# Optimization experiments

Hardware: AMD Instinct MI355X
Metric: run time of the kernel (lower is better)

The kernel has to match this reference:

```python
import jax, jax.numpy as jnp
import numpy as np


def setup_inputs() -> dict:
    key = jax.random.key(0)
    ks = jax.random.split(key, 5)
    B, T, I, H = 64, 2048, 128, 128
    bound = 1.0 / np.sqrt(H)
    x = jax.random.normal(ks[0], (B, T, I), dtype=jnp.float32)
    W_xh = jax.random.uniform(ks[1], (H, I), minval=-bound, maxval=bound, dtype=jnp.float32)
    b_xh = jax.random.uniform(ks[2], (H,), minval=-bound, maxval=bound, dtype=jnp.float32)
    W_hh = jax.random.uniform(ks[3], (H, H), minval=-bound, maxval=bound, dtype=jnp.float32)
    b_hh = jax.random.uniform(ks[4], (H,), minval=-bound, maxval=bound, dtype=jnp.float32)
    return {"x": x, "W_xh": W_xh, "b_xh": b_xh, "W_hh": W_hh, "b_hh": b_hh}


def reference(x, W_xh, b_xh, W_hh, b_hh):
    # x: [B, T, I]; nn.Linear applies x @ W.T + b.
    # Precompute the input projection for all timesteps in one GEMM.
    xp = jnp.einsum('bti,hi->bth', x, W_xh) + b_xh  # [B, T, H]
    B = x.shape[0]
    H = W_hh.shape[0]
    h0 = jnp.zeros((B, H), dtype=x.dtype)

    def step(h, xt):
        h_new = jnp.tanh(xt + h @ W_hh.T + b_hh)
        return h_new, h_new

    h_last, hs = jax.lax.scan(step, h0, jnp.swapaxes(xp, 0, 1))  # hs: [T, B, H]
    h_seq = jnp.swapaxes(hs, 0, 1)  # [B, T, H]
    return h_seq, h_last[None]  # h: [1, B, H]
```

## Files before the change

kernel.cpp:

```cpp
#include <hip/hip_runtime.h>

#define B_ 64
#define T_ 2048
#define I_ 128
#define H_ 128
#define CHUNK 128
#define NCHUNK (T_ / CHUNK)

typedef _Float16 f16x8 __attribute__((ext_vector_type(8)));
typedef float    f32x4 __attribute__((ext_vector_type(4)));
typedef int      i32x4 __attribute__((ext_vector_type(4)));

__global__ __launch_bounds__(256) void xp_gemm(
    const float* __restrict__ x, const float* __restrict__ Wxh,
    const float* __restrict__ bxh, const float* __restrict__ bhh,
    float* __restrict__ xp)
{
    __shared__ float ws[H_ * I_];
    const int tid = threadIdx.x;
    {
        const float4* src = (const float4*)Wxh;
        float4* dst = (float4*)ws;
        #pragma unroll
        for (int i = 0; i < (H_ * I_ / 4) / 256; ++i)
            dst[tid + i * 256] = src[tid + i * 256];
    }
    __syncthreads();

    const int r0 = (tid >> 4) * 8;
    const int c0 = (tid & 15) * 8;
    const float* xb = x + ((size_t)blockIdx.x * 128 + r0) * I_;
    const float* wb = ws + c0 * I_;

    float acc[8][8];
    #pragma unroll
    for (int i = 0; i < 8; ++i)
        #pragma unroll
        for (int j = 0; j < 8; ++j) acc[i][j] = 0.f;

    float4 xa[8], wa[8], xn[8], wn[8];
    #pragma unroll
    for (int i = 0; i < 8; ++i) xa[i] = *(const float4*)(xb + i * I_);
    #pragma unroll
    for (int j = 0; j < 8; ++j) wa[j] = *(const float4*)(wb + j * I_);

    for (int k4 = 0; k4 < 32; k4 += 2) {
        #pragma unroll
        for (int i = 0; i < 8; ++i) xn[i] = *(const float4*)(xb + i * I_ + k4 * 4 + 4);
        #pragma unroll
        for (int j = 0; j < 8; ++j) wn[j] = *(const float4*)(wb + j * I_ + k4 * 4 + 4);
        #pragma unroll
        for (int i = 0; i < 8; ++i)
            #pragma unroll
            for (int j = 0; j < 8; ++j) {
                acc[i][j] = fmaf(xa[i].x, wa[j].x, acc[i][j]);
                acc[i][j] = fmaf(xa[i].y, wa[j].y, acc[i][j]);
                acc[i][j] = fmaf(xa[i].z, wa[j].z, acc[i][j]);
                acc[i][j] = fmaf(xa[i].w, wa[j].w, acc[i][j]);
            }
        if (k4 + 2 < 32) {
            #pragma unroll
            for (int i = 0; i < 8; ++i) xa[i] = *(const float4*)(xb + i * I_ + k4 * 4 + 8);
            #pragma unroll
            for (int j = 0; j < 8; ++j) wa[j] = *(const float4*)(wb + j * I_ + k4 * 4 + 8);
        }
        #pragma unroll
        for (int i = 0; i < 8; ++i)
            #pragma unroll
            for (int j = 0; j < 8; ++j) {
                acc[i][j] = fmaf(xn[i].x, wn[j].x, acc[i][j]);
                acc[i][j] = fmaf(xn[i].y, wn[j].y, acc[i][j]);
                acc[i][j] = fmaf(xn[i].z, wn[j].z, acc[i][j]);
                acc[i][j] = fmaf(xn[i].w, wn[j].w, acc[i][j]);
            }
    }

    const float4 ba0 = *(const float4*)(bxh + c0);
    const float4 ba1 = *(const float4*)(bxh + c0 + 4);
    const float4 bb0 = *(const float4*)(bhh + c0);
    const float4 bb1 = *(const float4*)(bhh + c0 + 4);
    float* orow = xp + ((size_t)blockIdx.x * 128 + r0) * H_ + c0;
    #pragma unroll
    for (int i = 0; i < 8; ++i) {
        float4 o0, o1;
        o0.x = acc[i][0] + ba0.x + bb0.x; o0.y = acc[i][1] + ba0.y + bb0.y;
        o0.z = acc[i][2] + ba0.z + bb0.z; o0.w = acc[i][3] + ba0.w + bb0.w;
        o1.x = acc[i][4] + ba1.x + bb1.x; o1.y = acc[i][5] + ba1.y + bb1.y;
        o1.z = acc[i][6] + ba1.z + bb1.z; o1.w = acc[i][7] + ba1.w + bb1.w;
        *(float4*)(orow + i * H_) = o0;
        *(float4*)(orow + i * H_ + 4) = o1;
    }
}

__device__ __forceinline__ void stage_chunk64(const float* __restrict__ g,
                                              float* l, int ln)
{
    #pragma unroll
    for (int i = 0; i < 64; ++i) {
        const int off = i * 256;
        __builtin_amdgcn_global_load_lds(
            (const __attribute__((address_space(1))) unsigned int*)(g + off + ln * 4),
            (__attribute__((address_space(3))) unsigned int*)(l + off),
            16, 0, 0);
    }
}

#define FORALL(M) \
  M(0,0) M(1,0) M(2,0) M(3,0)  M(0,1) M(1,1) M(2,1) M(3,1) \
  M(0,2) M(1,2) M(2,2) M(3,2)  M(0,3) M(1,3) M(2,3) M(3,3) \
  M(0,4) M(1,4) M(2,4) M(3,4)  M(0,5) M(1,5) M(2,5) M(3,5) \
  M(0,6) M(1,6) M(2,6) M(3,6)  M(0,7) M(1,7) M(2,7) M(3,7)

#define DECLB(q,n) i32x4 bf_##q##_##n;
#define LOADB(q,n) { \
    const float* wr_ = Whh + (size_t)((n)*16 + c15) * H_ + (q)*32 + grp*8; \
    const float4 u0_ = *(const float4*)wr_; \
    const float4 u1_ = *(const float4*)(wr_ + 4); \
    f16x8 t_; \
    t_[0]=(_Float16)u0_.x; t_[1]=(_Float16)u0_.y; t_[2]=(_Float16)u0_.z; t_[3]=(_Float16)u0_.w; \
    t_[4]=(_Float16)u1_.x; t_[5]=(_Float16)u1_.y; t_[6]=(_Float16)u1_.z; t_[7]=(_Float16)u1_.w; \
    bf_##q##_##n = __builtin_bit_cast(i32x4, t_); }
#define PINB(q,n) asm volatile("" : "+a"(bf_##q##_##n));

#define FORN(M) M(0) M(1) M(2) M(3) M(4) M(5) M(6) M(7)
#define TILE(n) \
  f32x4 acc##n = __builtin_amdgcn_mfma_f32_16x16x32_f16(a0, __builtin_bit_cast(f16x8, bf_0_##n), zc, 0, 0, 0); \
  acc##n = __builtin_amdgcn_mfma_f32_16x16x32_f16(a1, __builtin_bit_cast(f16x8, bf_1_##n), acc##n, 0, 0, 0); \
  acc##n = __builtin_amdgcn_mfma_f32_16x16x32_f16(a2, __builtin_bit_cast(f16x8, bf_2_##n), acc##n, 0, 0, 0); \
  acc##n = __builtin_amdgcn_mfma_f32_16x16x32_f16(a3, __builtin_bit_cast(f16x8, bf_3_##n), acc##n, 0, 0, 0);

__global__ __launch_bounds__(64) void rnn_scan(
    const float* __restrict__ Whh,
    float* __restrict__ seq , float* __restrict__ hlast)
{
    __shared__ float xpl[2][CHUNK * H_];
    __shared__ _Float16 hA[H_], hB[H_];

    const int l   = threadIdx.x;
    const int b   = blockIdx.x;
    const int c15 = l & 15;
    const int grp = l >> 4;
    const int c0  = grp * 32 + c15;
    const int c1  = c0 + 16;

    FORALL(DECLB)
    FORALL(LOADB)
    FORALL(PINB)

    hA[2 * l] = (_Float16)0.f;
    hA[2 * l + 1] = (_Float16)0.f;

    const f32x4 zc = {0.f, 0.f, 0.f, 0.f};

    float* xp = seq + (size_t)b * T_ * H_;
    stage_chunk64(xp, &xpl[0][0], l);

    auto step = [&](const _Float16* hr, _Float16* hw,
                    const float* xrow, float* sqrow) {
        const float xv0 = xrow[c0];
        const float xv1 = xrow[c1];
        const f16x8 a0 = *(const f16x8*)(hr + grp * 8);
        const f16x8 a1 = *(const f16x8*)(hr + 32 + grp * 8);
        const f16x8 a2 = *(const f16x8*)(hr + 64 + grp * 8);
        const f16x8 a3 = *(const f16x8*)(hr + 96 + grp * 8);
        FORN(TILE)
        const float r0 = grp == 0 ? acc0.x : grp == 1 ? acc2.x : grp == 2 ? acc4.x : acc6.x;
        const float r1 = grp == 0 ? acc1.x : grp == 1 ? acc3.x : grp == 2 ? acc5.x : acc7.x;
        const float p0 = r0 + xv0;
        const float p1 = r1 + xv1;
        const float e0 = exp2f(p0 * 2.8853900817779268f);
        const float e1 = exp2f(p1 * 2.8853900817779268f);
        const float h0 = 1.f - 2.f * __builtin_amdgcn_rcpf(e0 + 1.f);
        const float h1 = 1.f - 2.f * __builtin_amdgcn_rcpf(e1 + 1.f);
        hw[c0] = (_Float16)h0;
        hw[c1] = (_Float16)h1;
        const float s0 = (float)hw[2 * l];
        const float s1 = (float)hw[2 * l + 1];
        *(float2*)(sqrow + 2 * l) = make_float2(s0, s1);
    };

    for (int c = 0; c < NCHUNK; ++c) {
        asm volatile("s_waitcnt vmcnt(0)" ::: "memory");
        if (c + 1 < NCHUNK)
            stage_chunk64(xp + (size_t)(c + 1) * CHUNK * H_, &xpl[(c + 1) & 1][0], l);

        const float* xb = &xpl[c & 1][0];
        float* sq = xp + (size_t)c * CHUNK * H_;

        for (int t = 0; t < CHUNK; t += 2) {
            step(hA, hB, xb + (size_t)t * H_, sq + (size_t)t * H_);
            step(hB, hA, xb + (size_t)(t + 1) * H_, sq + (size_t)(t + 1) * H_);
        }
    }
    const float f0 = (float)hA[2 * l];
    const float f1 = (float)hA[2 * l + 1];
    *(float2*)&hlast[b * H_ + 2 * l] = make_float2(f0, f1);
}

extern "C" void kernel_launch(void* const* d_in, const int* in_sizes, int n_in,
                              void* d_out, int out_size, void* d_ws, size_t ws_size,
                              hipStream_t stream)
{
    const float* x   = (const float*)d_in[0];
    const float* Wxh = (const float*)d_in[1];
    const float* bxh = (const float*)d_in[2];
    const float* Whh = (const float*)d_in[3];
    const float* bhh = (const float*)d_in[4];
    float* out   = (float*)d_out;
    float* hlast = out + (size_t)B_ * T_ * H_;

    xp_gemm<<<(B_ * T_) / 128, 256, 0, stream>>>(x, Wxh, bxh, bhh, out);
    rnn_scan<<<B_, 64, 0, stream>>>(Whh, out, hlast);
}
```

Measured before the change: 1.174 ms.

## Transpose recurrent MFMA so W_hh is A operand and accumulate into preloaded xp

The recurrent step now computes W_hh·h with W_hh in the A operand held in AGPRs, and h as a packed f16 B vector. xp rows are loaded straight into the MFMA accumulators, which removes the separate add. Each lane gets its two outputs through a fixed permutation (P/Lw), and a single packed 32-bit write into a tiny shared buffer carries h to the next step. The output is stored as fp32 without an f16 round trip, and the step loop is no longer unrolled by two. This aims to cut LDS traffic and scalar work on the serial critical path, at the cost of inline-asm register constraints and a complex index mapping.

```diff
diff --git a/kernel.cpp b/kernel.cpp
--- a/kernel.cpp
+++ b/kernel.cpp
@@ -7,9 +7,8 @@
 #define CHUNK 128
 #define NCHUNK (T_ / CHUNK)
 
-typedef _Float16 f16x8 __attribute__((ext_vector_type(8)));
-typedef float    f32x4 __attribute__((ext_vector_type(4)));
-typedef int      i32x4 __attribute__((ext_vector_type(4)));
+typedef float f32x4 __attribute__((ext_vector_type(4)));
+typedef int   i32x4 __attribute__((ext_vector_type(4)));
 
 __global__ __launch_bounds__(256) void xp_gemm(
     const float* __restrict__ x, const float* __restrict__ Wxh,
@@ -105,79 +104,52 @@
     }
 }
 
-#define FORALL(M) \
-  M(0,0) M(1,0) M(2,0) M(3,0)  M(0,1) M(1,1) M(2,1) M(3,1) \
-  M(0,2) M(1,2) M(2,2) M(3,2)  M(0,3) M(1,3) M(2,3) M(3,3) \
-  M(0,4) M(1,4) M(2,4) M(3,4)  M(0,5) M(1,5) M(2,5) M(3,5) \
-  M(0,6) M(1,6) M(2,6) M(3,6)  M(0,7) M(1,7) M(2,7) M(3,7)
-
-#define DECLB(q,n) i32x4 bf_##q##_##n;
-#define LOADB(q,n) { \
-    const float* wr_ = Whh + (size_t)((n)*16 + c15) * H_ + (q)*32 + grp*8; \
-    const float4 u0_ = *(const float4*)wr_; \
-    const float4 u1_ = *(const float4*)(wr_ + 4); \
-    f16x8 t_; \
-    t_[0]=(_Float16)u0_.x; t_[1]=(_Float16)u0_.y; t_[2]=(_Float16)u0_.z; t_[3]=(_Float16)u0_.w; \
-    t_[4]=(_Float16)u1_.x; t_[5]=(_Float16)u1_.y; t_[6]=(_Float16)u1_.z; t_[7]=(_Float16)u1_.w; \
-    bf_##q##_##n = __builtin_bit_cast(i32x4, t_); }
-#define PINB(q,n) asm volatile("" : "+a"(bf_##q##_##n));
-
-#define FORN(M) M(0) M(1) M(2) M(3) M(4) M(5) M(6) M(7)
-#define TILE(n) \
-  f32x4 acc##n = __builtin_amdgcn_mfma_f32_16x16x32_f16(a0, __builtin_bit_cast(f16x8, bf_0_##n), zc, 0, 0, 0); \
-  acc##n = __builtin_amdgcn_mfma_f32_16x16x32_f16(a1, __builtin_bit_cast(f16x8, bf_1_##n), acc##n, 0, 0, 0); \
-  acc##n = __builtin_amdgcn_mfma_f32_16x16x32_f16(a2, __builtin_bit_cast(f16x8, bf_2_##n), acc##n, 0, 0, 0); \
-  acc##n = __builtin_amdgcn_mfma_f32_16x16x32_f16(a3, __builtin_bit_cast(f16x8, bf_3_##n), acc##n, 0, 0, 0);
-
 __global__ __launch_bounds__(64) void rnn_scan(
     const float* __restrict__ Whh,
     float* __restrict__ seq , float* __restrict__ hlast)
 {
     __shared__ float xpl[2][CHUNK * H_];
-    __shared__ _Float16 hA[H_], hB[H_];
+    __shared__ unsigned hx[64];
 
     const int l   = threadIdx.x;
     const int b   = blockIdx.x;
     const int c15 = l & 15;
-    const int grp = l >> 4;
-    const int c0  = grp * 32 + c15;
-    const int c1  = c0 + 16;
-
-    FORALL(DECLB)
-    FORALL(LOADB)
-    FORALL(PINB)
-
-    hA[2 * l] = (_Float16)0.f;
-    hA[2 * l + 1] = (_Float16)0.f;
-
-    const f32x4 zc = {0.f, 0.f, 0.f, 0.f};
+    const int gp  = l >> 4;
+    const bool s1 = (c15 & 1);
+
+    i32x4 wA[8][4];
+    #pragma unroll
+    for (int m = 0; m < 8; ++m) {
+        const float* wr = Whh + (size_t)(16 * m + c15) * H_;
+        #pragma unroll
+        for (int q = 0; q < 4; ++q) {
+            const float4 u0 = *(const float4*)(wr + 32 * q + 8 * gp);
+            const float4 u1 = *(const float4*)(wr + 32 * q + 8 * gp + 4);
+            i32x4 t;
+            t.x = __builtin_bit_cast(int, __builtin_amdgcn_cvt_pkrtz(u0.x, u0.y));
+            t.y = __builtin_bit_cast(int, __builtin_amdgcn_cvt_pkrtz(u0.z, u0.w));
+            t.z = __builtin_bit_cast(int, __builtin_amdgcn_cvt_pkrtz(u1.x, u1.y));
+            t.w = __builtin_bit_cast(int, __builtin_amdgcn_cvt_pkrtz(u1.z, u1.w));
+            wA[m][q] = t;
+            asm("" : "+a"(wA[m][q]));
+        }
+    }
+
+    const int P     = 8 * (c15 >> 1) + 2 * gp + (c15 & 1);
+    const int Lw    = 16 * ((P >> 2) & 3) + 4 * (P >> 4) + (P & 3);
+    const int stoff = 2 * P;
+
+    hx[l] = 0u;
+    asm volatile("" ::: "memory");
+    const i32x4* hxv = (const i32x4*)hx;
+    i32x4 Bv0 = hxv[4 * gp + 0], Bv1 = hxv[4 * gp + 1],
+          Bv2 = hxv[4 * gp + 2], Bv3 = hxv[4 * gp + 3];
 
     float* xp = seq + (size_t)b * T_ * H_;
     stage_chunk64(xp, &xpl[0][0], l);
 
-    auto step = [&](const _Float16* hr, _Float16* hw,
-                    const float* xrow, float* sqrow) {
-        const float xv0 = xrow[c0];
-        const float xv1 = xrow[c1];
-        const f16x8 a0 = *(const f16x8*)(hr + grp * 8);
-        const f16x8 a1 = *(const f16x8*)(hr + 32 + grp * 8);
-        const f16x8 a2 = *(const f16x8*)(hr + 64 + grp * 8);
-        const f16x8 a3 = *(const f16x8*)(hr + 96 + grp * 8);
-        FORN(TILE)
-        const float r0 = grp == 0 ? acc0.x : grp == 1 ? acc2.x : grp == 2 ? acc4.x : acc6.x;
-        const float r1 = grp == 0 ? acc1.x : grp == 1 ? acc3.x : grp == 2 ? acc5.x : acc7.x;
-        const float p0 = r0 + xv0;
-        const float p1 = r1 + xv1;
-        const float e0 = exp2f(p0 * 2.8853900817779268f);
-        const float e1 = exp2f(p1 * 2.8853900817779268f);
-        const float h0 = 1.f - 2.f * __builtin_amdgcn_rcpf(e0 + 1.f);
-        const float h1 = 1.f - 2.f * __builtin_amdgcn_rcpf(e1 + 1.f);
-        hw[c0] = (_Float16)h0;
-        hw[c1] = (_Float16)h1;
-        const float s0 = (float)hw[2 * l];
-        const float s1 = (float)hw[2 * l + 1];
-        *(float2*)(sqrow + 2 * l) = make_float2(s0, s1);
-    };
+    f32x4 xa[8];
+    float h0v = 0.f, h1v = 0.f;
 
     for (int c = 0; c < NCHUNK; ++c) {
         asm volatile("s_waitcnt vmcnt(0)" ::: "memory");
@@ -186,15 +158,50 @@
 
         const float* xb = &xpl[c & 1][0];
         float* sq = xp + (size_t)c * CHUNK * H_;
-
-        for (int t = 0; t < CHUNK; t += 2) {
-            step(hA, hB, xb + (size_t)t * H_, sq + (size_t)t * H_);
-            step(hB, hA, xb + (size_t)(t + 1) * H_, sq + (size_t)(t + 1) * H_);
+        #pragma unroll
+        for (int m = 0; m < 8; ++m)
+            xa[m] = *(const f32x4*)(xb + 16 * m + 4 * gp);
+
+        for (int t = 0; t < CHUNK; ++t) {
+            #pragma unroll
+            for (int m = 0; m < 8; ++m) {
+                asm("v_mfma_f32_16x16x32_f16 %0, %1, %2, %0" : "+v"(xa[m]) : "a"(wA[m][0]), "v"(Bv0));
+                asm("v_mfma_f32_16x16x32_f16 %0, %1, %2, %0" : "+v"(xa[m]) : "a"(wA[m][1]), "v"(Bv1));
+                asm("v_mfma_f32_16x16x32_f16 %0, %1, %2, %0" : "+v"(xa[m]) : "a"(wA[m][2]), "v"(Bv2));
+                asm("v_mfma_f32_16x16x32_f16 %0, %1, %2, %0" : "+v"(xa[m]) : "a"(wA[m][3]), "v"(Bv3));
+            }
+            float e0[8], e1[8];
+            #pragma unroll
+            for (int m = 0; m < 8; ++m) {
+                e0[m] = s1 ? xa[m].z : xa[m].x;
+                e1[m] = s1 ? xa[m].w : xa[m].y;
+            }
+            float f0[4], f1[4];
+            #pragma unroll
+            for (int i = 0; i < 4; ++i) {
+                f0[i] = (c15 & 2) ? e0[2 * i + 1] : e0[2 * i];
+                f1[i] = (c15 & 2) ? e1[2 * i + 1] : e1[2 * i];
+            }
+            const float p0 = (c15 & 8) ? ((c15 & 4) ? f0[3] : f0[2])
+                                       : ((c15 & 4) ? f0[1] : f0[0]);
+            const float p1 = (c15 & 8) ? ((c15 & 4) ? f1[3] : f1[2])
+                                       : ((c15 & 4) ? f1[1] : f1[0]);
+            const float* nx = xb + (size_t)((t + 1 < CHUNK) ? t + 1 : t) * H_;
+            #pragma unroll
+            for (int m = 0; m < 8; ++m)
+                xa[m] = *(const f32x4*)(nx + 16 * m + 4 * gp);
+            const float q0 = exp2f(p0 * 2.8853900817779268f);
+            const float q1 = exp2f(p1 * 2.8853900817779268f);
+            h0v = 1.f - 2.f * __builtin_amdgcn_rcpf(q0 + 1.f);
+            h1v = 1.f - 2.f * __builtin_amdgcn_rcpf(q1 + 1.f);
+            hx[Lw] = __builtin_bit_cast(unsigned, __builtin_amdgcn_cvt_pkrtz(h0v, h1v));
+            asm volatile("" ::: "memory");
+            Bv0 = hxv[4 * gp + 0]; Bv1 = hxv[4 * gp + 1];
+            Bv2 = hxv[4 * gp + 2]; Bv3 = hxv[4 * gp + 3];
+            *(float2*)(sq + (size_t)t * H_ + stoff) = make_float2(h0v, h1v);
         }
     }
-    const float f0 = (float)hA[2 * l];
-    const float f1 = (float)hA[2 * l + 1];
-    *(float2*)&hlast[b * H_ + 2 * l] = make_float2(f0, f1);
+    *(float2*)&hlast[b * H_ + stoff] = make_float2(h0v, h1v);
 }
 
 extern "C" void kernel_launch(void* const* d_in, const int* in_sizes, int n_in,
```

Measured after the change: 1.393 ms. 18.6% more time.
